# Optimization experiments

Hardware: AMD Instinct MI355X
Metric: run time of the kernel (lower is better)

## Reference

```python
import jax, jax.numpy as jnp
import numpy as np

N = 40000      # nodes
E = 640000     # directed edges (avg degree 16)
IN_DIM = 64
HID = 64
OUT = 128
EPS_LN = 1e-5
EPS_BN = 1e-5
NEG_SLOPE = 0.2  # PyG GATConv default


def setup_inputs() -> dict:
    key = jax.random.key(0)
    ks = jax.random.split(key, 40)
    s = 0.05
    d = {}
    d["x"] = jax.random.normal(ks[0], (N, IN_DIM), jnp.float32)
    d["edge_index"] = jax.random.randint(ks[1], (2, E), 0, N, jnp.int32)
    d["pos"] = jax.random.normal(ks[2], (N, 3), jnp.float32)
    # GAT layer 1: in=64, out=64, heads=4 (concat)
    d["W1"] = jax.random.normal(ks[3], (4 * HID, IN_DIM), jnp.float32) * s
    d["a_s1"] = jax.random.normal(ks[4], (4, HID), jnp.float32) * s
    d["a_d1"] = jax.random.normal(ks[5], (4, HID), jnp.float32) * s
    d["bg1"] = jnp.zeros((4 * HID,), jnp.float32)
    d["ln1_g"] = jnp.ones((4 * HID,), jnp.float32)
    d["ln1_b"] = jnp.zeros((4 * HID,), jnp.float32)
    # GAT layer 2: in=256, out=64, heads=2 (concat)
    d["W2"] = jax.random.normal(ks[6], (2 * HID, 4 * HID), jnp.float32) * s
    d["a_s2"] = jax.random.normal(ks[7], (2, HID), jnp.float32) * s
    d["a_d2"] = jax.random.normal(ks[8], (2, HID), jnp.float32) * s
    d["bg2"] = jnp.zeros((2 * HID,), jnp.float32)
    d["ln2_g"] = jnp.ones((2 * HID,), jnp.float32)
    d["ln2_b"] = jnp.zeros((2 * HID,), jnp.float32)
    # GAT layer 3: in=128, out=128, heads=1
    d["W3"] = jax.random.normal(ks[9], (OUT, 2 * HID), jnp.float32) * s
    d["a_s3"] = jax.random.normal(ks[10], (1, OUT), jnp.float32) * s
    d["a_d3"] = jax.random.normal(ks[11], (1, OUT), jnp.float32) * s
    d["bg3"] = jnp.zeros((OUT,), jnp.float32)
    # pointnet: Conv1d(3,64,1) -> BN -> ReLU -> Conv1d(64,128,1) -> BN -> ReLU -> Conv1d(128,128,1)
    d["pw1"] = jax.random.normal(ks[12], (64, 3), jnp.float32) * s
    d["pb1"] = jnp.zeros((64,), jnp.float32)
    d["bn1_g"] = jnp.ones((64,), jnp.float32)
    d["bn1_b"] = jnp.zeros((64,), jnp.float32)
    d["pw2"] = jax.random.normal(ks[13], (128, 64), jnp.float32) * s
    d["pb2"] = jnp.zeros((128,), jnp.float32)
    d["bn2_g"] = jnp.ones((128,), jnp.float32)
    d["bn2_b"] = jnp.zeros((128,), jnp.float32)
    d["pw3"] = jax.random.normal(ks[14], (OUT, 128), jnp.float32) * s
    d["pb3"] = jnp.zeros((OUT,), jnp.float32)
    # fusion Linear(2*OUT, OUT)
    d["fw"] = jax.random.normal(ks[15], (OUT, 2 * OUT), jnp.float32) * s
    d["fb"] = jnp.zeros((OUT,), jnp.float32)
    return d


def _gat(x, W, a_s, a_d, b, src, dst, n):
    """PyG-style GATConv (concat=True, eval mode). x:[n,Fin], W:[H*C,Fin], a_*:[H,C]."""
    H, C = a_s.shape
    h = (x @ W.T).reshape(n, H, C)                       # [n,H,C]
    e_src = jnp.sum(h * a_s[None], -1)                   # [n,H]
    e_dst = jnp.sum(h * a_d[None], -1)                   # [n,H]
    e = jax.nn.leaky_relu(e_src[src] + e_dst[dst], NEG_SLOPE)   # [E,H]
    emax = jax.ops.segment_max(e, dst, num_segments=n)   # segment softmax over dst
    ex = jnp.exp(e - emax[dst])
    den = jax.ops.segment_sum(ex, dst, num_segments=n)
    alpha = ex / (den[dst] + 1e-16)                      # [E,H]
    out = jax.ops.segment_sum(alpha[:, :, None] * h[src], dst, num_segments=n)  # [n,H,C]
    return out.reshape(n, H * C) + b


def _ln(x, g, b):
    mu = jnp.mean(x, -1, keepdims=True)
    var = jnp.var(x, -1, keepdims=True)
    return (x - mu) * jax.lax.rsqrt(var + EPS_LN) * g + b


def _bn_eval(x, g, b):
    # eval-mode BatchNorm with freshly-initialized running stats (mean=0, var=1)
    return x * (g * jax.lax.rsqrt(jnp.float32(1.0 + EPS_BN))) + b


def reference(x, edge_index, pos, W1, a_s1, a_d1, bg1, ln1_g, ln1_b,
              W2, a_s2, a_d2, bg2, ln2_g, ln2_b, W3, a_s3, a_d3, bg3,
              pw1, pb1, bn1_g, bn1_b, pw2, pb2, bn2_g, bn2_b, pw3, pb3, fw, fb):
    n = x.shape[0]
    loops = jnp.arange(n, dtype=edge_index.dtype)        # PyG add_self_loops=True
    src = jnp.concatenate([edge_index[0], loops])
    dst = jnp.concatenate([edge_index[1], loops])

    x1 = jax.nn.relu(_ln(_gat(x, W1, a_s1, a_d1, bg1, src, dst, n), ln1_g, ln1_b))
    x2 = jax.nn.relu(_ln(_gat(x1, W2, a_s2, a_d2, bg2, src, dst, n), ln2_g, ln2_b))
    x3 = _gat(x2, W3, a_s3, a_d3, bg3, src, dst, n)      # [n,OUT]

    # pointnet: 1x1 conv1d == per-node linear
    p = jax.nn.relu(_bn_eval(pos @ pw1.T + pb1, bn1_g, bn1_b))
    p = jax.nn.relu(_bn_eval(p @ pw2.T + pb2, bn2_g, bn2_b))
    pos_features = p @ pw3.T + pb3                       # [n,OUT]

    combined = jnp.concatenate([x3, pos_features], -1)
    output = combined @ fw.T + fb
    return (output, x3, pos_features)
```

## Files before the change

### kernel.cpp

```cpp
#include <hip/hip_runtime.h>
#include <cstddef>

#define NNODES 40000
#define NEDGES 640000
#define NETOT  (NNODES + NEDGES)
#define ELLW   96
#define NCAST  30720
#define NBUCK  313
#define SEGCAP 8192
#define ABLOCKS 84
#define CBLOCKS 30

typedef unsigned short u16;
typedef unsigned int   u32;
using v2f = __attribute__((ext_vector_type(2))) float;

__device__ inline float wave_sum(float v) {
#pragma unroll
    for (int o = 32; o > 0; o >>= 1) v += __shfl_xor(v, o);
    return v;
}
__device__ inline u16 f2bf(float f) {
    u32 u = __float_as_uint(f);
    return (u16)((u + 0x7fffu + ((u >> 16) & 1u)) >> 16);
}

__global__ void build_a_kernel(const int* __restrict__ ei, u32* __restrict__ bcnt,
                               u32* __restrict__ seg,
                               const float* __restrict__ W1, const float* __restrict__ as1,
                               const float* __restrict__ ad1, float* __restrict__ vbuf,
                               const float* s0, u16* d0, int n0, const float* s1, u16* d1, int n1,
                               const float* s2, u16* d2, int n2, const float* s3, u16* d3, int n3,
                               const float* s4, u16* d4, int n4, const float* s5, u16* d5, int n5) {
    int tid = threadIdx.x;
    int blk = blockIdx.x;
    if (blk >= ABLOCKS) {
        if (blk < ABLOCKS + CBLOCKS) {
            int i = (blk - ABLOCKS) * 1024 + tid;
            const float* s; u16* d;
            if      (i < n0) { s = s0; d = d0; }
            else if ((i -= n0) < n1) { s = s1; d = d1; }
            else if ((i -= n1) < n2) { s = s2; d = d2; }
            else if ((i -= n2) < n3) { s = s3; d = d3; }
            else if ((i -= n3) < n4) { s = s4; d = d4; }
            else if ((i -= n4) < n5) { s = s5; d = d5; }
            else return;
            float4 v = ((const float4*)s)[i];
            ushort4 o; o.x = f2bf(v.x); o.y = f2bf(v.y); o.z = f2bf(v.z); o.w = f2bf(v.w);
            ((ushort4*)d)[i] = o;
        } else if (tid < 256) {
            int h = tid >> 6, k = tid & 63;
            float ss = 0.f, dd = 0.f;
            for (int c = 0; c < 64; c++) {
                float w = W1[(h * 64 + c) * 64 + k];
                ss += as1[h * 64 + c] * w;
                dd += ad1[h * 64 + c] * w;
            }
            vbuf[tid] = ss;
            vbuf[256 + tid] = dd;
        }
        return;
    }
    __shared__ u32 hist[NBUCK], hbase[NBUCK];
    for (int i = tid; i < NBUCK; i += 1024) hist[i] = 0;
    __syncthreads();
    u32 pk[8], loc[8]; int bj[8];
    int g0 = blk * 8192;
#pragma unroll
    for (int j = 0; j < 8; j++) {
        int g = g0 + j * 1024 + tid;
        bj[j] = -1;
        if (g < NETOT) {
            int src, dst;
            if (g < NEDGES) { src = ei[g]; dst = ei[NEDGES + g]; }
            else            { src = g - NEDGES; dst = src; }
            int b = dst >> 7;
            pk[j] = ((u32)dst << 16) | (u32)src;
            bj[j] = b;
            loc[j] = atomicAdd(&hist[b], 1u);
        }
    }
    __syncthreads();
    for (int i = tid; i < NBUCK; i += 1024) {
        u32 c = hist[i];
        hbase[i] = c ? atomicAdd(&bcnt[i], c) : 0u;
    }
    __syncthreads();
#pragma unroll
    for (int j = 0; j < 8; j++) {
        if (bj[j] >= 0) {
            u32 pos = hbase[bj[j]] + loc[j];
            if (pos < SEGCAP) seg[(size_t)bj[j] * SEGCAP + pos] = pk[j];
        }
    }
}

__global__ void build_b_kernel(const u32* __restrict__ seg, const u32* __restrict__ bcnt,
                               int* __restrict__ cnt, u16* __restrict__ srcs16,
                               int2* __restrict__ ovbuf) {
    __shared__ u32 lcnt[128];
    int tid = threadIdx.x;
    int b = blockIdx.x;
    int base = b << 7;
    if (tid < 128) lcnt[tid] = 0;
    __syncthreads();
    u32 m = bcnt[b]; if (m > SEGCAP) m = SEGCAP;
    const u32* sp = seg + (size_t)b * SEGCAP;
    for (u32 e = tid; e < m; e += 256) {
        u32 pkv = sp[e];
        u32 dst = pkv >> 16, src = pkv & 0xffffu;
        u32 p = atomicAdd(&lcnt[dst - (u32)base], 1u);
        if (p < ELLW) srcs16[dst * ELLW + p] = (u16)src;
        else {
            int q = atomicAdd(&cnt[NNODES], 1);
            ovbuf[q] = make_int2((int)dst, (int)src);
        }
    }
    __syncthreads();
    if (tid < 128 && base + tid < NNODES) cnt[base + tid] = (int)lcnt[tid];
}

__global__ void esed1_kernel(const float* __restrict__ x, const float* __restrict__ vbuf,
                             float* __restrict__ es, float* __restrict__ ed,
                             u16* __restrict__ xc) {
    __shared__ float vl[512];
    int tid = threadIdx.x;
    vl[tid] = vbuf[tid];
    vl[tid + 256] = vbuf[tid + 256];
    __syncthreads();
    int lane = tid & 63, wave = tid >> 6;
    int i = lane >> 2, q = lane & 3;
    int node = blockIdx.x * 64 + wave * 16 + i;
    const float* xp = x + (size_t)node * 64 + q * 16;
    float xr[16];
    *(float4*)&xr[0]  = ((const float4*)xp)[0];
    *(float4*)&xr[4]  = ((const float4*)xp)[1];
    *(float4*)&xr[8]  = ((const float4*)xp)[2];
    *(float4*)&xr[12] = ((const float4*)xp)[3];
    float p[8];
#pragma unroll
    for (int h = 0; h < 8; h++) {
        float s = 0.f;
#pragma unroll
        for (int j = 0; j < 16; j++) s += xr[j] * vl[h * 64 + q * 16 + j];
        p[h] = s;
    }
#pragma unroll
    for (int h = 0; h < 8; h++) {
        p[h] += __shfl_xor(p[h], 1);
        p[h] += __shfl_xor(p[h], 2);
    }
    es[node * 4 + q] = p[q];
    ed[node * 4 + q] = p[4 + q];
    u16* cp = xc + (size_t)node * 64 + q * 16;
#pragma unroll
    for (int j = 0; j < 16; j += 4) {
        ushort4 o; o.x = f2bf(xr[j]); o.y = f2bf(xr[j + 1]);
        o.z = f2bf(xr[j + 2]); o.w = f2bf(xr[j + 3]);
        *(ushort4*)(cp + j) = o;
    }
}

__global__ void gat_agg_kernel(const u16* __restrict__ xc,
                               const float* __restrict__ es, const float* __restrict__ ed,
                               const int* __restrict__ cnt, const u16* __restrict__ srcs16,
                               const int2* __restrict__ ovbuf,
                               u16* __restrict__ agg, int n) {
    __shared__ float wbuf[4][4][100];
    __shared__ u32   sbuf[4][ELLW];
    int wave = threadIdx.x >> 6;
    int wid = (blockIdx.x * blockDim.x + threadIdx.x) >> 6;
    int lane = threadIdx.x & 63;
    if (wid >= n) return;

    int degt = cnt[wid];
    int mainc = degt < ELLW ? degt : ELLW;
    int padt = (mainc + 7) & ~7;
    const u16* sp = srcs16 + (size_t)wid * ELLW;

    const int h = lane & 3;
    const int esub = lane >> 2;
    float edh = ed[(size_t)wid * 4 + h];

    float den = 0.f;
    for (int i0 = 0; i0 < padt; i0 += 16) {
        int e = i0 + esub;
        if (e < padt) {
            float w = 0.f; u32 off = 0;
            if (e < mainc) {
                int s = sp[e];
                off = (u32)s << 7;
                float v = es[(size_t)s * 4 + h] + edh;
                v = v > 0.f ? v : 0.2f * v;
                w = __expf(v);
            }
            wbuf[wave][h][e] = w;
            if (h == 0) sbuf[wave][e] = off;
            den += w;
        }
    }
    int ovn = 0;
    if (degt > ELLW) {
        ovn = cnt[n];
        for (int j = esub; j < ovn; j += 16) {
            int2 t = ovbuf[j];
            if (t.x == wid) {
                float v = es[(size_t)t.y * 4 + h] + edh;
                v = v > 0.f ? v : 0.2f * v;
                den += __expf(v);
            }
        }
    }
#pragma unroll
    for (int o = 4; o < 64; o <<= 1) den += __shfl_xor(den, o);
    float inv = 1.f / (den + 1e-16f);

    const int e2 = lane >> 5, f16 = lane & 31;
    const char* hp = (const char*)xc + f16 * 4;
    v2f a0 = {0.f, 0.f}, a1 = {0.f, 0.f}, a2 = {0.f, 0.f}, a3 = {0.f, 0.f};
    for (int eb = 0; eb < padt; eb += 8) {
        u32 of[4]; u32 g[4];
        float w0[4], w1[4], w2[4], w3[4];
#pragma unroll
        for (int k = 0; k < 4; k++) of[k] = sbuf[wave][eb + 2 * k + e2];
#pragma unroll
        for (int k = 0; k < 4; k++) g[k] = *(const u32*)(hp + of[k]);
#pragma unroll
        for (int k = 0; k < 4; k++) {
            int e = eb + 2 * k + e2;
            w0[k] = wbuf[wave][0][e]; w1[k] = wbuf[wave][1][e];
            w2[k] = wbuf[wave][2][e]; w3[k] = wbuf[wave][3][e];
        }
#pragma unroll
        for (int k = 0; k < 4; k++) {
            v2f hx;
            hx.x = __uint_as_float(g[k] << 16);
            hx.y = __uint_as_float(g[k] & 0xffff0000u);
            a0 += v2f{w0[k], w0[k]} * hx;
            a1 += v2f{w1[k], w1[k]} * hx;
            a2 += v2f{w2[k], w2[k]} * hx;
            a3 += v2f{w3[k], w3[k]} * hx;
        }
    }
    if (degt > ELLW) {
        for (int j = 0; j < ovn; j++) {
            int2 t = ovbuf[j];
            if (t.x != wid) continue;
            float wh[4];
#pragma unroll
            for (int hh = 0; hh < 4; hh++) {
                float v = es[(size_t)t.y * 4 + hh] + __shfl(edh, hh);
                v = v > 0.f ? v : 0.2f * v;
                wh[hh] = __expf(v);
            }
            if (lane < 32) {
                u32 g = *(const u32*)(hp + ((u32)t.y << 7));
                v2f hx;
                hx.x = __uint_as_float(g << 16);
                hx.y = __uint_as_float(g & 0xffff0000u);
                a0 += v2f{wh[0], wh[0]} * hx;
                a1 += v2f{wh[1], wh[1]} * hx;
                a2 += v2f{wh[2], wh[2]} * hx;
                a3 += v2f{wh[3], wh[3]} * hx;
            }
        }
    }
    a0.x += __shfl_xor(a0.x, 32); a0.y += __shfl_xor(a0.y, 32);
    a1.x += __shfl_xor(a1.x, 32); a1.y += __shfl_xor(a1.y, 32);
    a2.x += __shfl_xor(a2.x, 32); a2.y += __shfl_xor(a2.y, 32);
    a3.x += __shfl_xor(a3.x, 32); a3.y += __shfl_xor(a3.y, 32);
    float iv[4];
#pragma unroll
    for (int hh = 0; hh < 4; hh++) iv[hh] = __shfl(inv, hh);
    if (lane < 32) {
        u32* op = (u32*)agg + (size_t)wid * 128 + f16;
        op[0]  = ((u32)f2bf(a0.y * iv[0]) << 16) | f2bf(a0.x * iv[0]);
        op[32] = ((u32)f2bf(a1.y * iv[1]) << 16) | f2bf(a1.x * iv[1]);
        op[64] = ((u32)f2bf(a2.y * iv[2]) << 16) | f2bf(a2.x * iv[2]);
        op[96] = ((u32)f2bf(a3.y * iv[3]) << 16) | f2bf(a3.x * iv[3]);
    }
}

__global__ void w1ln_kernel(const u16* __restrict__ agg, const u16* __restrict__ B,
                            const float* __restrict__ bias,
                            const float* __restrict__ lng, const float* __restrict__ lnb,
                            u16* __restrict__ xb, int M) {
    using bfrag = __attribute__((ext_vector_type(8))) short;
    using ffrag = __attribute__((ext_vector_type(4))) float;
    int wave = threadIdx.x >> 6, lane = threadIdx.x & 63;
    int lm = lane & 15, kg = (lane >> 4) * 8;
    int rowblk = blockIdx.x * 64 + wave * 16;
    ffrag acc[16] = {};
#pragma unroll
    for (int hh = 0; hh < 4; hh++) {
#pragma unroll
        for (int k0 = 0; k0 < 64; k0 += 32) {
            bfrag af = *(const bfrag*)(agg + (size_t)(rowblk + lm) * 256 + hh * 64 + kg + k0);
#pragma unroll
            for (int tt = 0; tt < 4; tt++) {
                int t = hh * 4 + tt;
                bfrag bf = *(const bfrag*)(B + (size_t)(hh * 64 + tt * 16 + lm) * 64 + kg + k0);
                acc[t] = __builtin_amdgcn_mfma_f32_16x16x32_bf16(af, bf, acc[t], 0, 0, 0);
            }
        }
    }
    int orow = rowblk + (lane >> 4) * 4;
    float bi[16], gg[16], bb[16];
#pragma unroll
    for (int t = 0; t < 16; t++) {
        int col = t * 16 + lm;
        bi[t] = bias[col]; gg[t] = lng[col]; bb[t] = lnb[col];
    }
#pragma unroll
    for (int r = 0; r < 4; r++) {
        float pv[16];
        float s1 = 0.f, s2 = 0.f;
#pragma unroll
        for (int t = 0; t < 16; t++) {
            float v = acc[t][r] + bi[t];
            pv[t] = v; s1 += v; s2 += v * v;
        }
#pragma unroll
        for (int o = 1; o < 16; o <<= 1) { s1 += __shfl_xor(s1, o); s2 += __shfl_xor(s2, o); }
        float mu = s1 / 256.f;
        float var = s2 / 256.f - mu * mu;
        float rstd = rsqrtf(var + 1e-5f);
#pragma unroll
        for (int t = 0; t < 16; t++) {
            float v = (pv[t] - mu) * rstd * gg[t] + bb[t];
            v = v > 0.f ? v : 0.f;
            xb[(size_t)(orow + r) * 256 + t * 16 + lm] = f2bf(v);
        }
    }
}

template <int H, int C, bool AF32>
__global__ void gemm_scores_kernel(const void* __restrict__ Aptr, const u16* __restrict__ B,
                                   u16* __restrict__ Cout,
                                   const float* __restrict__ as, const float* __restrict__ ad,
                                   float* __restrict__ es, float* __restrict__ ed,
                                   int M, int Nn, int K) {
    constexpr int HT = 128 / C;
    using bfrag = __attribute__((ext_vector_type(8))) short;
    using ffrag = __attribute__((ext_vector_type(4))) float;
    int wave = threadIdx.x >> 6, lane = threadIdx.x & 63;
    int lm = lane & 15, kg = (lane >> 4) * 8;
    int rowblk = blockIdx.x * 64 + wave * 16;
    int n0 = blockIdx.y * 128;
    const u16* Bp = B + (size_t)(n0 + lm) * K + kg;
    ffrag acc[8] = {};
    for (int k0 = 0; k0 < K; k0 += 32) {
        bfrag af;
        if constexpr (AF32) {
            const float* ap = (const float*)Aptr + (size_t)(rowblk + lm) * K + kg + k0;
            float4 a0 = *(const float4*)ap;
            float4 a1 = *(const float4*)(ap + 4);
            af[0] = (short)f2bf(a0.x); af[1] = (short)f2bf(a0.y);
            af[2] = (short)f2bf(a0.z); af[3] = (short)f2bf(a0.w);
            af[4] = (short)f2bf(a1.x); af[5] = (short)f2bf(a1.y);
            af[6] = (short)f2bf(a1.z); af[7] = (short)f2bf(a1.w);
        } else {
            af = *(const bfrag*)((const u16*)Aptr + (size_t)(rowblk + lm) * K + kg + k0);
        }
#pragma unroll
        for (int t = 0; t < 8; t++) {
            bfrag bf = *(const bfrag*)(Bp + (size_t)t * 16 * K + k0);
            acc[t] = __builtin_amdgcn_mfma_f32_16x16x32_bf16(af, bf, acc[t], 0, 0, 0);
        }
    }
    int orow = rowblk + (lane >> 4) * 4;
    float asv[8], adv[8];
#pragma unroll
    for (int t = 0; t < 8; t++) {
        int fcol = n0 + t * 16 + lm;
        asv[t] = as[fcol]; adv[t] = ad[fcol];
    }
    float ps[4][HT] = {}, pd[4][HT] = {};
#pragma unroll
    for (int t = 0; t < 8; t++) {
        const int hh = t / (C / 16);
#pragma unroll
        for (int r = 0; r < 4; r++) {
            float v = acc[t][r];
            ps[r][hh] += v * asv[t];
            pd[r][hh] += v * adv[t];
            Cout[(size_t)(orow + r) * Nn + n0 + t * 16 + lm] = f2bf(v);
        }
    }
    int hb = blockIdx.y * HT;
#pragma unroll
    for (int r = 0; r < 4; r++)
#pragma unroll
        for (int hh = 0; hh < HT; hh++) {
            float s = ps[r][hh], d = pd[r][hh];
#pragma unroll
            for (int o = 1; o < 16; o <<= 1) { s += __shfl_xor(s, o); d += __shfl_xor(d, o); }
            if (lm == 0) {
                es[(size_t)(orow + r) * H + hb + hh] = s;
                ed[(size_t)(orow + r) * H + hb + hh] = d;
            }
        }
}

template <int H, int C, bool LNRELU>
__global__ void gat_fused_kernel(const u16* __restrict__ hmat,
                                 const float* __restrict__ es, const float* __restrict__ ed,
                                 const int* __restrict__ cnt, const u16* __restrict__ srcs16,
                                 const int2* __restrict__ ovbuf,
                                 const float* __restrict__ bias,
                                 const float* __restrict__ lng, const float* __restrict__ lnb,
                                 void* __restrict__ out, int n) {
    constexpr int HC = H * C;
    constexpr int VPT = HC / 64;
    constexpr int SH = (HC == 256) ? 9 : 8;
    constexpr int EPW = 64 / H;
    constexpr int HSH = (H == 4) ? 2 : ((H == 2) ? 1 : 0);
    __shared__ float wbuf[4][H][100];
    __shared__ int   sbuf[4][ELLW];
    int wave = threadIdx.x >> 6;
    int wid = (blockIdx.x * blockDim.x + threadIdx.x) >> 6;
    int lane = threadIdx.x & 63;
    if (wid >= n) return;

    int degt = cnt[wid];
    int mainc = degt < ELLW ? degt : ELLW;
    int pad = (mainc + 7) & ~7;
    const u16* sp = srcs16 + (size_t)wid * ELLW;

    const int h = lane & (H - 1);
    const int esub = lane >> HSH;
    float edh = ed[(size_t)wid * H + h];

    float den = 0.f;
    for (int i0 = 0; i0 < pad; i0 += EPW) {
        int e = i0 + esub;
        if (e < pad) {
            float w = 0.f;
            int soff = 0;
            if (e < mainc) {
                int s = sp[e];
                soff = s << SH;
                float v = es[(size_t)s * H + h] + edh;
                v = v > 0.f ? v : 0.2f * v;
                w = __expf(v);
            }
            wbuf[wave][h][e] = w;
            if (h == 0) sbuf[wave][e] = soff;
            den += w;
        }
    }
    int ovn = 0;
    if (degt > ELLW) {
        ovn = cnt[n];
        for (int j = esub; j < ovn; j += EPW) {
            int2 t = ovbuf[j];
            if (t.x == wid) {
                float v = es[(size_t)t.y * H + h] + edh;
                v = v > 0.f ? v : 0.2f * v;
                den += __expf(v);
            }
        }
    }
#pragma unroll
    for (int o = H; o < 64; o <<= 1) den += __shfl_xor(den, o);
    float inv = 1.f / (den + 1e-16f);

    const int myhead = (lane * VPT) / C;
    const float invh = __shfl(inv, myhead);
    const int loff = lane * (VPT * 2);
    v2f a01 = {0.f, 0.f}, a23 = {0.f, 0.f};

    for (int e = 0; e < pad; e += 8) {
        int4   o0 = *(const int4*)&sbuf[wave][e];
        int4   o1 = *(const int4*)&sbuf[wave][e + 4];
        float4 w0 = *(const float4*)&wbuf[wave][myhead][e];
        float4 w1 = *(const float4*)&wbuf[wave][myhead][e + 4];
        int   oo[8] = {o0.x, o0.y, o0.z, o0.w, o1.x, o1.y, o1.z, o1.w};
        float ww[8] = {w0.x, w0.y, w0.z, w0.w, w1.x, w1.y, w1.z, w1.w};
        if constexpr (VPT == 4) {
            uint2 gg[8];
#pragma unroll
            for (int u = 0; u < 8; u++)
                gg[u] = *(const uint2*)((const char*)hmat + (size_t)(u32)oo[u] + loff);
#pragma unroll
            for (int u = 0; u < 8; u++) {
                v2f wv = {ww[u], ww[u]};
                v2f h01, h23;
                h01.x = __uint_as_float(gg[u].x << 16);
                h01.y = __uint_as_float(gg[u].x & 0xffff0000u);
                h23.x = __uint_as_float(gg[u].y << 16);
                h23.y = __uint_as_float(gg[u].y & 0xffff0000u);
                a01 += wv * h01;
                a23 += wv * h23;
            }
        } else {
            u32 gg[8];
#pragma unroll
            for (int u = 0; u < 8; u++)
                gg[u] = *(const u32*)((const char*)hmat + (size_t)(u32)oo[u] + loff);
#pragma unroll
            for (int u = 0; u < 8; u++) {
                v2f wv = {ww[u], ww[u]};
                v2f h01;
                h01.x = __uint_as_float(gg[u] << 16);
                h01.y = __uint_as_float(gg[u] & 0xffff0000u);
                a01 += wv * h01;
            }
        }
    }
    if (degt > ELLW) {
        const float edm = __shfl(edh, myhead);
        for (int j = 0; j < ovn; j++) {
            int2 t = ovbuf[j];
            if (t.x != wid) continue;
            float v = es[(size_t)t.y * H + myhead] + edm;
            v = v > 0.f ? v : 0.2f * v;
            float w = __expf(v);
            v2f wv = {w, w};
            if constexpr (VPT == 4) {
                uint2 g = *(const uint2*)((const char*)hmat + ((size_t)t.y << SH) + loff);
                v2f h01, h23;
                h01.x = __uint_as_float(g.x << 16);
                h01.y = __uint_as_float(g.x & 0xffff0000u);
                h23.x = __uint_as_float(g.y << 16);
                h23.y = __uint_as_float(g.y & 0xffff0000u);
                a01 += wv * h01;
                a23 += wv * h23;
            } else {
                u32 g = *(const u32*)((const char*)hmat + ((size_t)t.y << SH) + loff);
                v2f h01;
                h01.x = __uint_as_float(g << 16);
                h01.y = __uint_as_float(g & 0xffff0000u);
                a01 += wv * h01;
            }
        }
    }
    {
        v2f iv = {invh, invh};
        a01 *= iv;
        a23 *= iv;
    }

    int fbase = lane * VPT;
    float y[VPT];
    y[0] = a01.x + bias[fbase + 0];
    y[1] = a01.y + bias[fbase + 1];
    if constexpr (VPT == 4) {
        y[2] = a23.x + bias[fbase + 2];
        y[3] = a23.y + bias[fbase + 3];
    }

    if constexpr (LNRELU) {
        float s1 = 0.f, s2 = 0.f;
#pragma unroll
        for (int j = 0; j < VPT; j++) { s1 += y[j]; s2 += y[j] * y[j]; }
        s1 = wave_sum(s1);
        s2 = wave_sum(s2);
        float mu = s1 / (float)HC;
        float var = s2 / (float)HC - mu * mu;
        float rstd = rsqrtf(var + 1e-5f);
#pragma unroll
        for (int j = 0; j < VPT; j++) {
            float v = (y[j] - mu) * rstd * lng[fbase + j] + lnb[fbase + j];
            y[j] = v > 0.f ? v : 0.f;
        }
        u16* op = (u16*)out + (size_t)wid * HC + fbase;
        if constexpr (VPT == 4) {
            ushort4 o; o.x = f2bf(y[0]); o.y = f2bf(y[1]); o.z = f2bf(y[2]); o.w = f2bf(y[3]);
            *(ushort4*)op = o;
        } else {
            ushort2 o; o.x = f2bf(y[0]); o.y = f2bf(y[1]);
            *(ushort2*)op = o;
        }
    } else {
        float* op = (float*)out + (size_t)wid * HC + fbase;
        if constexpr (VPT == 4) *(float4*)op = make_float4(y[0], y[1], y[2], y[3]);
        else                    *(float2*)op = make_float2(y[0], y[1]);
    }
}

__global__ void gemm_pn12_kernel(const float* __restrict__ pos,
                                 const float* __restrict__ pw1, const float* __restrict__ pb1,
                                 const float* __restrict__ bn1g, const float* __restrict__ bn1b,
                                 const u16* __restrict__ B, u16* __restrict__ Cout,
                                 const float* __restrict__ pb2,
                                 const float* __restrict__ bn2g, const float* __restrict__ bn2b,
                                 int M) {
    const int Nn = 128, K = 64;
    using bfrag = __attribute__((ext_vector_type(8))) short;
    using ffrag = __attribute__((ext_vector_type(4))) float;
    int wave = threadIdx.x >> 6, lane = threadIdx.x & 63;
    int lm = lane & 15, kg = (lane >> 4) * 8;
    int rowblk = blockIdx.x * 64 + wave * 16;
    int row = rowblk + lm;
    float p0 = pos[row * 3 + 0], p1 = pos[row * 3 + 1], p2 = pos[row * 3 + 2];
    const u16* Bp = B + (size_t)lm * K + kg;
    const float bnscale = rsqrtf(1.0f + 1e-5f);
    ffrag acc[8] = {};
#pragma unroll
    for (int k0 = 0; k0 < K; k0 += 32) {
        bfrag af;
#pragma unroll
        for (int j = 0; j < 8; j++) {
            int k = kg + k0 + j;
            float v = p0 * pw1[k * 3 + 0] + p1 * pw1[k * 3 + 1] + p2 * pw1[k * 3 + 2] + pb1[k];
            v = v * (bn1g[k] * bnscale) + bn1b[k];
            v = v > 0.f ? v : 0.f;
            af[j] = (short)f2bf(v);
        }
#pragma unroll
        for (int t = 0; t < 8; t++) {
            bfrag bf = *(const bfrag*)(Bp + (size_t)t * 16 * K + k0);
            acc[t] = __builtin_amdgcn_mfma_f32_16x16x32_bf16(af, bf, acc[t], 0, 0, 0);
        }
    }
    int orow = rowblk + (lane >> 4) * 4;
#pragma unroll
    for (int t = 0; t < 8; t++) {
        int col = t * 16 + lm;
        float bi = pb2[col], g = bn2g[col] * bnscale, bb = bn2b[col];
#pragma unroll
        for (int r = 0; r < 4; r++) {
            float v = (acc[t][r] + bi) * g + bb;
            v = v > 0.f ? v : 0.f;
            Cout[(size_t)(orow + r) * Nn + col] = f2bf(v);
        }
    }
}

__global__ void gemm_pw3cat_kernel(const u16* __restrict__ p2, const u16* __restrict__ Bpw3,
                                   const float* __restrict__ pb3, float* __restrict__ pf,
                                   const float* __restrict__ x3, const u16* __restrict__ Bfw,
                                   const float* __restrict__ fb, float* __restrict__ outp,
                                   int M) {
    using bfrag = __attribute__((ext_vector_type(8))) short;
    using ffrag = __attribute__((ext_vector_type(4))) float;
    __shared__ float pft[64][132];
    int wave = threadIdx.x >> 6, lane = threadIdx.x & 63;
    int lm = lane & 15, kg = (lane >> 4) * 8;
    int rowblk = blockIdx.x * 64 + wave * 16;
    int rowbase = blockIdx.x * 64;

    {
        const u16* Ap = p2 + (size_t)(rowblk + lm) * 128 + kg;
        const u16* Bp = Bpw3 + (size_t)lm * 128 + kg;
        ffrag acc[8] = {};
#pragma unroll
        for (int k0 = 0; k0 < 128; k0 += 32) {
            bfrag af = *(const bfrag*)(Ap + k0);
#pragma unroll
            for (int t = 0; t < 8; t++) {
                bfrag bf = *(const bfrag*)(Bp + (size_t)t * 16 * 128 + k0);
                acc[t] = __builtin_amdgcn_mfma_f32_16x16x32_bf16(af, bf, acc[t], 0, 0, 0);
            }
        }
        int lrow = wave * 16 + (lane >> 4) * 4;
#pragma unroll
        for (int t = 0; t < 8; t++) {
            int col = t * 16 + lm;
            float bi = pb3[col];
#pragma unroll
            for (int r = 0; r < 4; r++)
                pft[lrow + r][col] = acc[t][r] + bi;
        }
    }
    __syncthreads();

    for (int i = threadIdx.x; i < 2048; i += 256) {
        int row = i >> 5, c4 = (i & 31) << 2;
        float4 v = *(const float4*)&pft[row][c4];
        *(float4*)&pf[(size_t)(rowbase + row) * 128 + c4] = v;
    }

    {
        const u16* Bp = Bfw + (size_t)lm * 256 + kg;
        ffrag acc[8] = {};
        int row = rowblk + lm, lrow = wave * 16 + lm;
#pragma unroll
        for (int k0 = 0; k0 < 256; k0 += 32) {
            bfrag af;
            if (k0 < 128) {
                const float* ap = x3 + (size_t)row * 128 + kg + k0;
                float4 a0 = *(const float4*)ap;
                float4 a1 = *(const float4*)(ap + 4);
                af[0] = (short)f2bf(a0.x); af[1] = (short)f2bf(a0.y);
                af[2] = (short)f2bf(a0.z); af[3] = (short)f2bf(a0.w);
                af[4] = (short)f2bf(a1.x); af[5] = (short)f2bf(a1.y);
                af[6] = (short)f2bf(a1.z); af[7] = (short)f2bf(a1.w);
            } else {
                const float* ap = &pft[lrow][kg + k0 - 128];
                float4 a0 = *(const float4*)ap;
                float4 a1 = *(const float4*)(ap + 4);
                af[0] = (short)f2bf(a0.x); af[1] = (short)f2bf(a0.y);
                af[2] = (short)f2bf(a0.z); af[3] = (short)f2bf(a0.w);
                af[4] = (short)f2bf(a1.x); af[5] = (short)f2bf(a1.y);
                af[6] = (short)f2bf(a1.z); af[7] = (short)f2bf(a1.w);
            }
#pragma unroll
            for (int t = 0; t < 8; t++) {
                bfrag bf = *(const bfrag*)(Bp + (size_t)t * 16 * 256 + k0);
                acc[t] = __builtin_amdgcn_mfma_f32_16x16x32_bf16(af, bf, acc[t], 0, 0, 0);
            }
        }
        __syncthreads();
        int lrow2 = wave * 16 + (lane >> 4) * 4;
#pragma unroll
        for (int t = 0; t < 8; t++) {
            int col = t * 16 + lm;
            float bi = fb[col];
#pragma unroll
            for (int r = 0; r < 4; r++)
                pft[lrow2 + r][col] = acc[t][r] + bi;
        }
        __syncthreads();
        for (int i = threadIdx.x; i < 2048; i += 256) {
            int rw = i >> 5, c4 = (i & 31) << 2;
            float4 v = *(const float4*)&pft[rw][c4];
            *(float4*)&outp[(size_t)(rowbase + rw) * 128 + c4] = v;
        }
    }
}

extern "C" void kernel_launch(void* const* d_in, const int* in_sizes, int n_in,
                              void* d_out, int out_size, void* d_ws, size_t ws_size,
                              hipStream_t stream) {
    const float* x    = (const float*)d_in[0];
    const int*   ei   = (const int*)d_in[1];
    const float* pos  = (const float*)d_in[2];
    const float* W1   = (const float*)d_in[3];
    const float* as1  = (const float*)d_in[4];
    const float* ad1  = (const float*)d_in[5];
    const float* bg1  = (const float*)d_in[6];
    const float* ln1g = (const float*)d_in[7];
    const float* ln1b = (const float*)d_in[8];
    const float* W2   = (const float*)d_in[9];
    const float* as2  = (const float*)d_in[10];
    const float* ad2  = (const float*)d_in[11];
    const float* bg2  = (const float*)d_in[12];
    const float* ln2g = (const float*)d_in[13];
    const float* ln2b = (const float*)d_in[14];
    const float* W3   = (const float*)d_in[15];
    const float* as3  = (const float*)d_in[16];
    const float* ad3  = (const float*)d_in[17];
    const float* bg3  = (const float*)d_in[18];
    const float* pw1  = (const float*)d_in[19];
    const float* pb1  = (const float*)d_in[20];
    const float* bn1g = (const float*)d_in[21];
    const float* bn1b = (const float*)d_in[22];
    const float* pw2  = (const float*)d_in[23];
    const float* pb2  = (const float*)d_in[24];
    const float* bn2g = (const float*)d_in[25];
    const float* bn2b = (const float*)d_in[26];
    const float* pw3  = (const float*)d_in[27];
    const float* pb3  = (const float*)d_in[28];
    const float* fw   = (const float*)d_in[29];
    const float* fb   = (const float*)d_in[30];

    const int N = NNODES;
    float* out = (float*)d_out;
    float* x3  = out + (size_t)N * 128;
    float* pf  = out + (size_t)2 * N * 128;

    char* ws = (char*)d_ws;
    size_t off = 0;
    auto alloc = [&](size_t bytes) -> void* {
        void* p = ws + off;
        off += (bytes + 255) / 256 * 256;
        return p;
    };
    int*   cnt    = (int*)alloc((size_t)(N + 1 + NBUCK) * 4);
    u32*   bcnt   = (u32*)(cnt + N + 1);
    u32*   seg    = (u32*)alloc((size_t)NBUCK * SEGCAP * 4);
    u16*   srcs16 = (u16*)alloc((size_t)N * ELLW * 2);
    int2*  ovbuf  = (int2*)alloc((size_t)NETOT * 8);
    float* esb    = (float*)alloc((size_t)N * 4 * 4);
    float* edb    = (float*)alloc((size_t)N * 4 * 4);
    u16*   w1c    = (u16*)alloc(16384 * 2);
    u16*   w2c    = (u16*)alloc(32768 * 2);
    u16*   w3c    = (u16*)alloc(16384 * 2);
    u16*   pw2c   = (u16*)alloc(8192 * 2);
    u16*   pw3c   = (u16*)alloc(16384 * 2);
    u16*   fwc    = (u16*)alloc(32768 * 2);
    u16*   hbufb  = (u16*)alloc((size_t)N * 128 * 2);
    u16*   xb     = (u16*)alloc((size_t)N * 256 * 2);
    u16*   p2b    = (u16*)alloc((size_t)N * 128 * 2);
    u16*   xc     = (u16*)alloc((size_t)N * 64 * 2);
    float* vbuf   = (float*)alloc(512 * 4);
    u16*   aggb   = (u16*)alloc((size_t)N * 256 * 2);

    hipMemsetAsync(cnt, 0, (size_t)(N + 1 + NBUCK) * 4, stream);
    build_a_kernel<<<ABLOCKS + CBLOCKS + 1, 1024, 0, stream>>>(
        ei, bcnt, seg, W1, as1, ad1, vbuf,
        W1, w1c, 4096, W2, w2c, 8192, W3, w3c, 4096,
        pw2, pw2c, 2048, pw3, pw3c, 4096, fw, fwc, 8192);
    build_b_kernel<<<NBUCK, 256, 0, stream>>>(seg, bcnt, cnt, srcs16, ovbuf);

    const int NW = N / 4;
    const int GB = N / 64;

    gemm_pn12_kernel<<<GB, 256, 0, stream>>>(
        pos, pw1, pb1, bn1g, bn1b, pw2c, p2b, pb2, bn2g, bn2b, N);

    esed1_kernel<<<GB, 256, 0, stream>>>(x, vbuf, esb, edb, xc);
    gat_agg_kernel<<<NW, 256, 0, stream>>>(xc, esb, edb, cnt, srcs16, ovbuf, aggb, N);
    w1ln_kernel<<<GB, 256, 0, stream>>>(aggb, w1c, bg1, ln1g, ln1b, xb, N);

    gemm_scores_kernel<2, 64, false><<<dim3(GB, 1), 256, 0, stream>>>(
        xb, w2c, hbufb, as2, ad2, esb, edb, N, 128, 256);
    gat_fused_kernel<2, 64, true><<<NW, 256, 0, stream>>>(
        hbufb, esb, edb, cnt, srcs16, ovbuf, bg2, ln2g, ln2b, xb, N);

    gemm_scores_kernel<1, 128, false><<<dim3(GB, 1), 256, 0, stream>>>(
        xb, w3c, hbufb, as3, ad3, esb, edb, N, 128, 128);
    gat_fused_kernel<1, 128, false><<<NW, 256, 0, stream>>>(
        hbufb, esb, edb, cnt, srcs16, ovbuf, bg3, nullptr, nullptr, x3, N);

    gemm_pw3cat_kernel<<<GB, 256, 0, stream>>>(p2b, pw3c, pb3, pf, x3, fwc, fb, out, N);
}
```

Measured before the change: 359.5 us.

## Merge independent build, score and pointnet stages into one launch; widen final GEMM

Three independent kernels (ELL bucket scatter, layer-1 score/bf16 cast, and the pointnet first two layers) are merged into one launch that dispatches on block index, cutting two launches and letting the stages overlap on the GPU. The final pw3+fusion GEMM kernel now uses 512 threads, with the eight waves splitting the 128 output columns into two halves, so each wave holds fewer accumulators and each block has more parallelism. The merged kernel's register and LDS footprint is the maximum over its branches, which may lower occupancy for the lighter branches.

```diff
diff --git a/kernel.cpp b/kernel.cpp
--- a/kernel.cpp
+++ b/kernel.cpp
@@ -10,6 +10,7 @@
 #define SEGCAP 8192
 #define ABLOCKS 84
 #define CBLOCKS 30
+#define GBLK   625
 
 typedef unsigned short u16;
 typedef unsigned int   u32;
@@ -95,69 +96,122 @@
     }
 }
 
-__global__ void build_b_kernel(const u32* __restrict__ seg, const u32* __restrict__ bcnt,
-                               int* __restrict__ cnt, u16* __restrict__ srcs16,
-                               int2* __restrict__ ovbuf) {
+__global__ void mid_kernel(const u32* __restrict__ seg, const u32* __restrict__ bcnt,
+                           int* __restrict__ cnt, u16* __restrict__ srcs16,
+                           int2* __restrict__ ovbuf,
+                           const float* __restrict__ x, const float* __restrict__ vbuf,
+                           float* __restrict__ es, float* __restrict__ ed, u16* __restrict__ xc,
+                           const float* __restrict__ pos,
+                           const float* __restrict__ pw1, const float* __restrict__ pb1,
+                           const float* __restrict__ bn1g, const float* __restrict__ bn1b,
+                           const u16* __restrict__ Bpn, u16* __restrict__ p2out,
+                           const float* __restrict__ pb2,
+                           const float* __restrict__ bn2g, const float* __restrict__ bn2b) {
     __shared__ u32 lcnt[128];
-    int tid = threadIdx.x;
-    int b = blockIdx.x;
-    int base = b << 7;
-    if (tid < 128) lcnt[tid] = 0;
-    __syncthreads();
-    u32 m = bcnt[b]; if (m > SEGCAP) m = SEGCAP;
-    const u32* sp = seg + (size_t)b * SEGCAP;
-    for (u32 e = tid; e < m; e += 256) {
-        u32 pkv = sp[e];
-        u32 dst = pkv >> 16, src = pkv & 0xffffu;
-        u32 p = atomicAdd(&lcnt[dst - (u32)base], 1u);
-        if (p < ELLW) srcs16[dst * ELLW + p] = (u16)src;
-        else {
-            int q = atomicAdd(&cnt[NNODES], 1);
-            ovbuf[q] = make_int2((int)dst, (int)src);
-        }
-    }
-    __syncthreads();
-    if (tid < 128 && base + tid < NNODES) cnt[base + tid] = (int)lcnt[tid];
-}
-
-__global__ void esed1_kernel(const float* __restrict__ x, const float* __restrict__ vbuf,
-                             float* __restrict__ es, float* __restrict__ ed,
-                             u16* __restrict__ xc) {
     __shared__ float vl[512];
     int tid = threadIdx.x;
-    vl[tid] = vbuf[tid];
-    vl[tid + 256] = vbuf[tid + 256];
-    __syncthreads();
-    int lane = tid & 63, wave = tid >> 6;
-    int i = lane >> 2, q = lane & 3;
-    int node = blockIdx.x * 64 + wave * 16 + i;
-    const float* xp = x + (size_t)node * 64 + q * 16;
-    float xr[16];
-    *(float4*)&xr[0]  = ((const float4*)xp)[0];
-    *(float4*)&xr[4]  = ((const float4*)xp)[1];
-    *(float4*)&xr[8]  = ((const float4*)xp)[2];
-    *(float4*)&xr[12] = ((const float4*)xp)[3];
-    float p[8];
-#pragma unroll
-    for (int h = 0; h < 8; h++) {
-        float s = 0.f;
-#pragma unroll
-        for (int j = 0; j < 16; j++) s += xr[j] * vl[h * 64 + q * 16 + j];
-        p[h] = s;
-    }
-#pragma unroll
-    for (int h = 0; h < 8; h++) {
-        p[h] += __shfl_xor(p[h], 1);
-        p[h] += __shfl_xor(p[h], 2);
-    }
-    es[node * 4 + q] = p[q];
-    ed[node * 4 + q] = p[4 + q];
-    u16* cp = xc + (size_t)node * 64 + q * 16;
-#pragma unroll
-    for (int j = 0; j < 16; j += 4) {
-        ushort4 o; o.x = f2bf(xr[j]); o.y = f2bf(xr[j + 1]);
-        o.z = f2bf(xr[j + 2]); o.w = f2bf(xr[j + 3]);
-        *(ushort4*)(cp + j) = o;
+    int blk = blockIdx.x;
+
+    if (blk < NBUCK) {
+        int base = blk << 7;
+        if (tid < 128) lcnt[tid] = 0;
+        __syncthreads();
+        u32 m = bcnt[blk]; if (m > SEGCAP) m = SEGCAP;
+        const u32* sp = seg + (size_t)blk * SEGCAP;
+        for (u32 e = tid; e < m; e += 256) {
+            u32 pkv = sp[e];
+            u32 dst = pkv >> 16, src = pkv & 0xffffu;
+            u32 p = atomicAdd(&lcnt[dst - (u32)base], 1u);
+            if (p < ELLW) srcs16[dst * ELLW + p] = (u16)src;
+            else {
+                int q = atomicAdd(&cnt[NNODES], 1);
+                ovbuf[q] = make_int2((int)dst, (int)src);
+            }
+        }
+        __syncthreads();
+        if (tid < 128 && base + tid < NNODES) cnt[base + tid] = (int)lcnt[tid];
+        return;
+    }
+    blk -= NBUCK;
+    if (blk < GBLK) {
+        vl[tid] = vbuf[tid];
+        vl[tid + 256] = vbuf[tid + 256];
+        __syncthreads();
+        int lane = tid & 63, wave = tid >> 6;
+        int i = lane >> 2, q = lane & 3;
+        int node = blk * 64 + wave * 16 + i;
+        const float* xp = x + (size_t)node * 64 + q * 16;
+        float xr[16];
+        *(float4*)&xr[0]  = ((const float4*)xp)[0];
+        *(float4*)&xr[4]  = ((const float4*)xp)[1];
+        *(float4*)&xr[8]  = ((const float4*)xp)[2];
+        *(float4*)&xr[12] = ((const float4*)xp)[3];
+        float p[8];
+#pragma unroll
+        for (int h = 0; h < 8; h++) {
+            float s = 0.f;
+#pragma unroll
+            for (int j = 0; j < 16; j++) s += xr[j] * vl[h * 64 + q * 16 + j];
+            p[h] = s;
+        }
+#pragma unroll
+        for (int h = 0; h < 8; h++) {
+            p[h] += __shfl_xor(p[h], 1);
+            p[h] += __shfl_xor(p[h], 2);
+        }
+        es[node * 4 + q] = p[q];
+        ed[node * 4 + q] = p[4 + q];
+        u16* cp = xc + (size_t)node * 64 + q * 16;
+#pragma unroll
+        for (int j = 0; j < 16; j += 4) {
+            ushort4 o; o.x = f2bf(xr[j]); o.y = f2bf(xr[j + 1]);
+            o.z = f2bf(xr[j + 2]); o.w = f2bf(xr[j + 3]);
+            *(ushort4*)(cp + j) = o;
+        }
+        return;
+    }
+    blk -= GBLK;
+    {
+        const int Nn = 128, K = 64;
+        using bfrag = __attribute__((ext_vector_type(8))) short;
+        using ffrag = __attribute__((ext_vector_type(4))) float;
+        int wave = tid >> 6, lane = tid & 63;
+        int lm = lane & 15, kg = (lane >> 4) * 8;
+        int rowblk = blk * 64 + wave * 16;
+        int row = rowblk + lm;
+        float p0 = pos[row * 3 + 0], p1 = pos[row * 3 + 1], p2 = pos[row * 3 + 2];
+        const u16* Bp = Bpn + (size_t)lm * K + kg;
+        const float bnscale = rsqrtf(1.0f + 1e-5f);
+        ffrag acc[8] = {};
+#pragma unroll
+        for (int k0 = 0; k0 < K; k0 += 32) {
+            bfrag af;
+#pragma unroll
+            for (int j = 0; j < 8; j++) {
+                int k = kg + k0 + j;
+                float v = p0 * pw1[k * 3 + 0] + p1 * pw1[k * 3 + 1] + p2 * pw1[k * 3 + 2] + pb1[k];
+                v = v * (bn1g[k] * bnscale) + bn1b[k];
+                v = v > 0.f ? v : 0.f;
+                af[j] = (short)f2bf(v);
+            }
+#pragma unroll
+            for (int t = 0; t < 8; t++) {
+                bfrag bf = *(const bfrag*)(Bp + (size_t)t * 16 * K + k0);
+                acc[t] = __builtin_amdgcn_mfma_f32_16x16x32_bf16(af, bf, acc[t], 0, 0, 0);
+            }
+        }
+        int orow = rowblk + (lane >> 4) * 4;
+#pragma unroll
+        for (int t = 0; t < 8; t++) {
+            int col = t * 16 + lm;
+            float bi = pb2[col], g = bn2g[col] * bnscale, bb = bn2b[col];
+#pragma unroll
+            for (int r = 0; r < 4; r++) {
+                float v = (acc[t][r] + bi) * g + bb;
+                v = v > 0.f ? v : 0.f;
+                p2out[(size_t)(orow + r) * Nn + col] = f2bf(v);
+            }
+        }
     }
 }
 
@@ -579,55 +633,6 @@
     }
 }
 
-__global__ void gemm_pn12_kernel(const float* __restrict__ pos,
-                                 const float* __restrict__ pw1, const float* __restrict__ pb1,
-                                 const float* __restrict__ bn1g, const float* __restrict__ bn1b,
-                                 const u16* __restrict__ B, u16* __restrict__ Cout,
-                                 const float* __restrict__ pb2,
-                                 const float* __restrict__ bn2g, const float* __restrict__ bn2b,
-                                 int M) {
-    const int Nn = 128, K = 64;
-    using bfrag = __attribute__((ext_vector_type(8))) short;
-    using ffrag = __attribute__((ext_vector_type(4))) float;
-    int wave = threadIdx.x >> 6, lane = threadIdx.x & 63;
-    int lm = lane & 15, kg = (lane >> 4) * 8;
-    int rowblk = blockIdx.x * 64 + wave * 16;
-    int row = rowblk + lm;
-    float p0 = pos[row * 3 + 0], p1 = pos[row * 3 + 1], p2 = pos[row * 3 + 2];
-    const u16* Bp = B + (size_t)lm * K + kg;
-    const float bnscale = rsqrtf(1.0f + 1e-5f);
-    ffrag acc[8] = {};
-#pragma unroll
-    for (int k0 = 0; k0 < K; k0 += 32) {
-        bfrag af;
-#pragma unroll
-        for (int j = 0; j < 8; j++) {
-            int k = kg + k0 + j;
-            float v = p0 * pw1[k * 3 + 0] + p1 * pw1[k * 3 + 1] + p2 * pw1[k * 3 + 2] + pb1[k];
-            v = v * (bn1g[k] * bnscale) + bn1b[k];
-            v = v > 0.f ? v : 0.f;
-            af[j] = (short)f2bf(v);
-        }
-#pragma unroll
-        for (int t = 0; t < 8; t++) {
-            bfrag bf = *(const bfrag*)(Bp + (size_t)t * 16 * K + k0);
-            acc[t] = __builtin_amdgcn_mfma_f32_16x16x32_bf16(af, bf, acc[t], 0, 0, 0);
-        }
-    }
-    int orow = rowblk + (lane >> 4) * 4;
-#pragma unroll
-    for (int t = 0; t < 8; t++) {
-        int col = t * 16 + lm;
-        float bi = pb2[col], g = bn2g[col] * bnscale, bb = bn2b[col];
-#pragma unroll
-        for (int r = 0; r < 4; r++) {
-            float v = (acc[t][r] + bi) * g + bb;
-            v = v > 0.f ? v : 0.f;
-            Cout[(size_t)(orow + r) * Nn + col] = f2bf(v);
-        }
-    }
-}
-
 __global__ void gemm_pw3cat_kernel(const u16* __restrict__ p2, const u16* __restrict__ Bpw3,
                                    const float* __restrict__ pb3, float* __restrict__ pf,
                                    const float* __restrict__ x3, const u16* __restrict__ Bfw,
@@ -638,26 +643,28 @@
     __shared__ float pft[64][132];
     int wave = threadIdx.x >> 6, lane = threadIdx.x & 63;
     int lm = lane & 15, kg = (lane >> 4) * 8;
-    int rowblk = blockIdx.x * 64 + wave * 16;
+    int rw = wave & 3, ch = wave >> 2;
+    int rowblk = blockIdx.x * 64 + rw * 16;
     int rowbase = blockIdx.x * 64;
+    int colbase = ch * 64;
 
     {
         const u16* Ap = p2 + (size_t)(rowblk + lm) * 128 + kg;
-        const u16* Bp = Bpw3 + (size_t)lm * 128 + kg;
-        ffrag acc[8] = {};
+        const u16* Bp = Bpw3 + (size_t)(colbase + lm) * 128 + kg;
+        ffrag acc[4] = {};
 #pragma unroll
         for (int k0 = 0; k0 < 128; k0 += 32) {
             bfrag af = *(const bfrag*)(Ap + k0);
 #pragma unroll
-            for (int t = 0; t < 8; t++) {
+            for (int t = 0; t < 4; t++) {
                 bfrag bf = *(const bfrag*)(Bp + (size_t)t * 16 * 128 + k0);
                 acc[t] = __builtin_amdgcn_mfma_f32_16x16x32_bf16(af, bf, acc[t], 0, 0, 0);
             }
         }
-        int lrow = wave * 16 + (lane >> 4) * 4;
-#pragma unroll
-        for (int t = 0; t < 8; t++) {
-            int col = t * 16 + lm;
+        int lrow = rw * 16 + (lane >> 4) * 4;
+#pragma unroll
+        for (int t = 0; t < 4; t++) {
+            int col = colbase + t * 16 + lm;
             float bi = pb3[col];
 #pragma unroll
             for (int r = 0; r < 4; r++)
@@ -666,16 +673,16 @@
     }
     __syncthreads();
 
-    for (int i = threadIdx.x; i < 2048; i += 256) {
+    for (int i = threadIdx.x; i < 2048; i += 512) {
         int row = i >> 5, c4 = (i & 31) << 2;
         float4 v = *(const float4*)&pft[row][c4];
         *(float4*)&pf[(size_t)(rowbase + row) * 128 + c4] = v;
     }
 
     {
-        const u16* Bp = Bfw + (size_t)lm * 256 + kg;
-        ffrag acc[8] = {};
-        int row = rowblk + lm, lrow = wave * 16 + lm;
+        const u16* Bp = Bfw + (size_t)(colbase + lm) * 256 + kg;
+        ffrag acc[4] = {};
+        int row = rowblk + lm, lrow = rw * 16 + lm;
 #pragma unroll
         for (int k0 = 0; k0 < 256; k0 += 32) {
             bfrag af;
@@ -697,26 +704,26 @@
                 af[6] = (short)f2bf(a1.z); af[7] = (short)f2bf(a1.w);
             }
 #pragma unroll
-            for (int t = 0; t < 8; t++) {
+            for (int t = 0; t < 4; t++) {
                 bfrag bf = *(const bfrag*)(Bp + (size_t)t * 16 * 256 + k0);
                 acc[t] = __builtin_amdgcn_mfma_f32_16x16x32_bf16(af, bf, acc[t], 0, 0, 0);
             }
         }
         __syncthreads();
-        int lrow2 = wave * 16 + (lane >> 4) * 4;
-#pragma unroll
-        for (int t = 0; t < 8; t++) {
-            int col = t * 16 + lm;
+        int lrow2 = rw * 16 + (lane >> 4) * 4;
+#pragma unroll
+        for (int t = 0; t < 4; t++) {
+            int col = colbase + t * 16 + lm;
             float bi = fb[col];
 #pragma unroll
             for (int r = 0; r < 4; r++)
                 pft[lrow2 + r][col] = acc[t][r] + bi;
         }
         __syncthreads();
-        for (int i = threadIdx.x; i < 2048; i += 256) {
-            int rw = i >> 5, c4 = (i & 31) << 2;
-            float4 v = *(const float4*)&pft[rw][c4];
-            *(float4*)&outp[(size_t)(rowbase + rw) * 128 + c4] = v;
+        for (int i = threadIdx.x; i < 2048; i += 512) {
+            int rw2 = i >> 5, c4 = (i & 31) << 2;
+            float4 v = *(const float4*)&pft[rw2][c4];
+            *(float4*)&outp[(size_t)(rowbase + rw2) * 128 + c4] = v;
         }
     }
 }
@@ -793,15 +800,15 @@
         ei, bcnt, seg, W1, as1, ad1, vbuf,
         W1, w1c, 4096, W2, w2c, 8192, W3, w3c, 4096,
         pw2, pw2c, 2048, pw3, pw3c, 4096, fw, fwc, 8192);
-    build_b_kernel<<<NBUCK, 256, 0, stream>>>(seg, bcnt, cnt, srcs16, ovbuf);
+
+    mid_kernel<<<NBUCK + 2 * GBLK, 256, 0, stream>>>(
+        seg, bcnt, cnt, srcs16, ovbuf,
+        x, vbuf, esb, edb, xc,
+        pos, pw1, pb1, bn1g, bn1b, pw2c, p2b, pb2, bn2g, bn2b);
 
     const int NW = N / 4;
-    const int GB = N / 64;
-
-    gemm_pn12_kernel<<<GB, 256, 0, stream>>>(
-        pos, pw1, pb1, bn1g, bn1b, pw2c, p2b, pb2, bn2g, bn2b, N);
-
-    esed1_kernel<<<GB, 256, 0, stream>>>(x, vbuf, esb, edb, xc);
+    const int GB = GBLK;
+
     gat_agg_kernel<<<NW, 256, 0, stream>>>(xc, esb, edb, cnt, srcs16, ovbuf, aggb, N);
     w1ln_kernel<<<GB, 256, 0, stream>>>(aggb, w1c, bg1, ln1g, ln1b, xb, N);
 
@@ -815,5 +822,5 @@
     gat_fused_kernel<1, 128, false><<<NW, 256, 0, stream>>>(
         hbufb, esb, edb, cnt, srcs16, ovbuf, bg3, nullptr, nullptr, x3, N);
 
-    gemm_pw3cat_kernel<<<GB, 256, 0, stream>>>(p2b, pw3c, pb3, pf, x3, fwc, fb, out, N);
-}
+    gemm_pw3cat_kernel<<<GB, 512, 0, stream>>>(p2b, pw3c, pb3, pf, x3, fwc, fb, out, N);
+}
```

Measured after the change: 354.1 us. No clear change (-1.5%).
